# Optimization experiments

Measured on AMD Instinct MI355X. Metric: run time of the kernel, lower is better.

Reference implementation:

```python
import jax, jax.numpy as jnp
import numpy as np

N = 100000
IN_DIM = 128
OUT_DIM = 128
E = 320000


def setup_inputs() -> dict:
    key = jax.random.key(0)
    ks = jax.random.split(key, 12)
    x = jax.random.normal(ks[0], (N, IN_DIM), dtype=jnp.float32)
    src0 = jax.random.randint(ks[1], (E,), 0, N)
    dst0 = jax.random.randint(ks[2], (E,), 0, N)
    src1 = jax.random.randint(ks[3], (E,), 0, N)
    dst1 = jax.random.randint(ks[4], (E,), 0, N)
    s = 1.0 / np.sqrt(IN_DIM)
    W0 = jax.random.uniform(ks[5], (IN_DIM, OUT_DIM), minval=-s, maxval=s)
    b0 = jax.random.uniform(ks[6], (OUT_DIM,), minval=-s, maxval=s)
    W1 = jax.random.uniform(ks[7], (IN_DIM, OUT_DIM), minval=-s, maxval=s)
    b1 = jax.random.uniform(ks[8], (OUT_DIM,), minval=-s, maxval=s)
    sa = 1.0 / np.sqrt(2 * OUT_DIM)
    a0 = jax.random.uniform(ks[9], (2 * OUT_DIM,), minval=-sa, maxval=sa)
    a1 = jax.random.uniform(ks[10], (2 * OUT_DIM,), minval=-sa, maxval=sa)
    return {"x": x, "src0": src0, "dst0": dst0, "src1": src1, "dst1": dst1,
            "W0": W0, "b0": b0, "a0": a0, "W1": W1, "b1": b1, "a1": a1}


def _rel_gat(x, src, dst, W, b, a):
    # wh = Linear(in_dim, out_dim)(x)  -> [N, D]
    wh = x @ W + b
    D = wh.shape[1]
    # e = leaky_relu(a^T [wh_src || wh_dst]) ; split a instead of concat on edges
    e = jax.nn.leaky_relu(wh[src] @ a[:D] + wh[dst] @ a[D:])  # [E]
    # segment softmax over incoming edges of each dst node
    m = jax.ops.segment_max(e, dst, num_segments=N)
    ex = jnp.exp(e - m[dst])
    denom = jax.ops.segment_sum(ex, dst, num_segments=N)
    alpha = ex / denom[dst]  # [E]
    # weighted scatter-sum of src features (zero for isolated dst nodes)
    return jax.ops.segment_sum(alpha[:, None] * wh[src], dst, num_segments=N)


def reference(x, src0, dst0, src1, dst1, W0, b0, a0, W1, b1, a1):
    h0 = _rel_gat(x, src0, dst0, W0, b0, a0)
    h1 = _rel_gat(x, src1, dst1, W1, b1, a1)
    # cross-relation 'sum' reducer
    return h0 + h1
```

## Files before the change

### kernel.cpp

```cpp
#include <hip/hip_runtime.h>
#include <hip/hip_bf16.h>


typedef __bf16 bf16x8 __attribute__((ext_vector_type(8)));
typedef float f32x4 __attribute__((ext_vector_type(4)));

#define DIM 128
#define SPREAD 16

__global__ __launch_bounds__(256) void prep_w_kernel(
    const float* __restrict__ W0, const float* __restrict__ W1,
    __bf16* __restrict__ wtf)
{
    const int e = blockIdx.x * 256 + threadIdx.x;
    if (e >= 4096) return;
    const int lane = e & 63;
    const int ko4  = (e >> 6) & 3;
    const int ct   = (e >> 8) & 7;
    const int rel  = e >> 11;
    const float* W = rel ? W1 : W0;
    const int n  = ct * 16 + (lane & 15);
    const int k0 = ko4 * 32 + (lane >> 4) * 8;
    bf16x8 v;
#pragma unroll
    for (int j = 0; j < 8; ++j) v[j] = (__bf16)W[(k0 + j) * DIM + n];
    *(bf16x8*)(wtf + (size_t)e * 8) = v;
}

__global__ __launch_bounds__(256) void gemm_wh_kernel(
    const float* __restrict__ x, const __bf16* __restrict__ wtf,
    const float* __restrict__ b0, const float* __restrict__ b1,
    const float* __restrict__ a0, const float* __restrict__ a1,
    const int* __restrict__ dst0, const int* __restrict__ dst1,
    unsigned* __restrict__ deg, unsigned* __restrict__ rank,
    __bf16* __restrict__ wh, float* __restrict__ s_src,
    float* __restrict__ s_dst, int N, int E)
{
    __shared__ __align__(16) __bf16 Cst[64 * 136];
    const int tid = threadIdx.x;

    {
        const int gid = blockIdx.x * 256 + tid;
        if (gid < E) {
            rank[gid]     = atomicAdd(deg + (size_t)dst0[gid] * SPREAD, 1u);
            rank[E + gid] = atomicAdd(deg + ((size_t)N + dst1[gid]) * SPREAD, 1u);
        }
    }

    const int lane = tid & 63;
    const int wave = tid >> 6;
    const int quad = lane >> 4;
    const int mr   = lane & 15;

    const long row0 = (long)blockIdx.x * 64 + wave * 16;
    long arow = row0 + mr;
    if (arow >= N) arow = N - 1;
    const f32x4* xr = (const f32x4*)(x + arow * DIM);

    bf16x8 afrag[4];
#pragma unroll
    for (int ko4 = 0; ko4 < 4; ++ko4) {
        f32x4 lo = xr[ko4 * 8 + quad * 2], hi = xr[ko4 * 8 + quad * 2 + 1];
        afrag[ko4] = (bf16x8){ (__bf16)lo.x, (__bf16)lo.y, (__bf16)lo.z, (__bf16)lo.w,
                               (__bf16)hi.x, (__bf16)hi.y, (__bf16)hi.z, (__bf16)hi.w };
    }

    const bf16x8* wt = (const bf16x8*)wtf;

#pragma unroll
    for (int rel = 0; rel < 2; ++rel) {
        f32x4 zero = {0.f, 0.f, 0.f, 0.f};
        f32x4 acc[8];
#pragma unroll
        for (int t = 0; t < 8; ++t) acc[t] = zero;

#pragma unroll
        for (int ko4 = 0; ko4 < 4; ++ko4) {
#pragma unroll
            for (int ct = 0; ct < 8; ++ct) {
                bf16x8 bfrag = wt[((rel * 8 + ct) * 4 + ko4) * 64 + lane];
                acc[ct] = __builtin_amdgcn_mfma_f32_16x16x32_bf16(afrag[ko4], bfrag, acc[ct], 0, 0, 0);
            }
        }

        const float* bias = rel ? b1 : b0;
        const float* a    = rel ? a1 : a0;
        float psr[4] = {0.f, 0.f, 0.f, 0.f};
        float pdr[4] = {0.f, 0.f, 0.f, 0.f};
#pragma unroll
        for (int ct = 0; ct < 8; ++ct) {
            const int c = ct * 16 + mr;
            const float bn = bias[c];
            const float asc = a[c], adc = a[DIM + c];
#pragma unroll
            for (int rr = 0; rr < 4; ++rr) {
                const float wv = acc[ct][rr] + bn;
                Cst[(wave * 16 + quad * 4 + rr) * 136 + c] = (__bf16)wv;
                psr[rr] += asc * wv;
                pdr[rr] += adc * wv;
            }
        }
#pragma unroll
        for (int off = 1; off < 16; off <<= 1) {
#pragma unroll
            for (int rr = 0; rr < 4; ++rr) {
                psr[rr] += __shfl_xor(psr[rr], off);
                pdr[rr] += __shfl_xor(pdr[rr], off);
            }
        }
        if (mr == 0) {
#pragma unroll
            for (int rr = 0; rr < 4; ++rr) {
                const long orow = row0 + quad * 4 + rr;
                if (orow < N) {
                    s_src[(size_t)rel * N + orow] = psr[rr];
                    s_dst[(size_t)rel * N + orow] = pdr[rr];
                }
            }
        }
        __syncthreads();
#pragma unroll
        for (int i = 0; i < 4; ++i) {
            const int chunk = tid + 256 * i;
            const int row = chunk >> 4, c8 = chunk & 15;
            bf16x8 v = *(const bf16x8*)&Cst[row * 136 + c8 * 8];
            const long grow = (long)blockIdx.x * 64 + row;
            if (grow < N)
                *(bf16x8*)(wh + ((size_t)rel * N + grow) * DIM + c8 * 8) = v;
        }
        __syncthreads();
    }
}

__global__ __launch_bounds__(256) void scanA_kernel(
    const unsigned* __restrict__ deg, unsigned* __restrict__ tmp,
    unsigned* __restrict__ bsum, int n)
{
    __shared__ unsigned s[256];
    const int t = threadIdx.x;
    const int i = blockIdx.x * 256 + t;
    unsigned v = (i < n) ? deg[(size_t)i * SPREAD] : 0u;
    s[t] = v;
    __syncthreads();
#pragma unroll
    for (int off = 1; off < 256; off <<= 1) {
        unsigned add = (t >= off) ? s[t - off] : 0u;
        __syncthreads();
        s[t] += add;
        __syncthreads();
    }
    if (i < n) tmp[i] = s[t] - v;
    if (t == 255) bsum[blockIdx.x] = s[t];
}

__global__ __launch_bounds__(256) void scan2_kernel(
    const unsigned* __restrict__ tmp, const unsigned* __restrict__ bsum,
    const unsigned* __restrict__ deg, unsigned* __restrict__ rowptr,
    int n, int nb)
{
    __shared__ unsigned s[256];
    __shared__ unsigned ex[1024];
    const int t = threadIdx.x;
    unsigned loc[4], sum = 0u;
#pragma unroll
    for (int k = 0; k < 4; ++k) {
        int idx = t * 4 + k;
        loc[k] = (idx < nb) ? bsum[idx] : 0u;
        sum += loc[k];
    }
    s[t] = sum;
    __syncthreads();
#pragma unroll
    for (int off = 1; off < 256; off <<= 1) {
        unsigned add = (t >= off) ? s[t - off] : 0u;
        __syncthreads();
        s[t] += add;
        __syncthreads();
    }
    unsigned run = s[t] - sum;
#pragma unroll
    for (int k = 0; k < 4; ++k) {
        ex[t * 4 + k] = run;
        run += loc[k];
    }
    __syncthreads();
    const unsigned pref = ex[blockIdx.x];
    const int i = blockIdx.x * 256 + t;
    if (i < n) {
        unsigned val = tmp[i] + pref;
        rowptr[i] = val;
        if (i == n - 1) rowptr[n] = val + deg[(size_t)i * SPREAD];
    }
}

__global__ __launch_bounds__(256) void fill_kernel(
    const int* __restrict__ src0, const int* __restrict__ dst0,
    const int* __restrict__ src1, const int* __restrict__ dst1,
    const float* __restrict__ s_src, const float* __restrict__ s_dst,
    const unsigned* __restrict__ rowptr, const unsigned* __restrict__ rank,
    uint2* __restrict__ sorted, int N, int E)
{
    const int i = blockIdx.x * 256 + threadIdx.x;
    if (i >= E) return;
    const int s0 = src0[i], d0 = dst0[i];
    const int s1 = src1[i], d1 = dst1[i];
    const unsigned p0 = rowptr[d0] + rank[i];
    const unsigned p1 = rowptr[N + d1] + rank[E + i];

    float v0 = s_src[s0] + s_dst[d0];
    v0 = v0 > 0.f ? v0 : 0.01f * v0;
    const float e0 = __expf(v0);
    float v1 = s_src[N + s1] + s_dst[N + d1];
    v1 = v1 > 0.f ? v1 : 0.01f * v1;
    const float e1 = __expf(v1);

    sorted[p0] = make_uint2((unsigned)s0, __float_as_uint(e0));
    sorted[p1] = make_uint2((unsigned)s1, __float_as_uint(e1));
}

__global__ __launch_bounds__(256) void aggregate_kernel(
    const unsigned* __restrict__ rowptr, const uint2* __restrict__ sorted,
    const __bf16* __restrict__ wh, float* __restrict__ out, int N)
{
    const int tid  = threadIdx.x;
    const int lane = tid & 63;
    const int sub  = lane >> 4;
    const int mr   = lane & 15;
    int d = blockIdx.x * 4 + (tid >> 6);
    if (d >= N) return;
    d = __builtin_amdgcn_readfirstlane(d);

    const unsigned beg0 = rowptr[d],     end0 = rowptr[d + 1];
    const unsigned beg1 = rowptr[N + d], end1 = rowptr[N + d + 1];
    const unsigned len0 = end0 - beg0;
    const unsigned T    = len0 + (end1 - beg1);

    float acc0[8], acc1[8], l0 = 0.f, l1 = 0.f;
#pragma unroll
    for (int k = 0; k < 8; ++k) { acc0[k] = 0.f; acc1[k] = 0.f; }

    const size_t whstride = (size_t)N * DIM;

    for (unsigned t0 = 0; t0 < T; t0 += 8) {
        const unsigned tA = t0 + sub, tB = tA + 4;
        const bool vA = tA < T, vB = tB < T;
        const bool rA = tA >= len0, rB = tB >= len0;

        unsigned iA = rA ? beg1 + (tA - len0) : beg0 + tA;
        unsigned iB = rB ? beg1 + (tB - len0) : beg0 + tB;
        iA = vA ? iA : 0u;
        iB = vB ? iB : 0u;

        const uint2 eA = sorted[iA];
        const uint2 eB = sorted[iB];

        const float evA = vA ? __uint_as_float(eA.y) : 0.f;
        const float evB = vB ? __uint_as_float(eB.y) : 0.f;
        const float wA0 = rA ? 0.f : evA, wA1 = rA ? evA : 0.f;
        const float wB0 = rB ? 0.f : evB, wB1 = rB ? evB : 0.f;
        l0 += wA0 + wB0;
        l1 += wA1 + wB1;

        const bf16x8 wA = *(const bf16x8*)(wh + (rA ? whstride : 0)
                                              + (size_t)eA.x * DIM + mr * 8);
        const bf16x8 wB = *(const bf16x8*)(wh + (rB ? whstride : 0)
                                              + (size_t)eB.x * DIM + mr * 8);
#pragma unroll
        for (int k = 0; k < 8; ++k) {
            const float fA = (float)wA[k], fB = (float)wB[k];
            acc0[k] += wA0 * fA + wB0 * fB;
            acc1[k] += wA1 * fA + wB1 * fB;
        }
    }

#pragma unroll
    for (int k = 0; k < 8; ++k) {
        acc0[k] += __shfl_xor(acc0[k], 16);
        acc0[k] += __shfl_xor(acc0[k], 32);
        acc1[k] += __shfl_xor(acc1[k], 16);
        acc1[k] += __shfl_xor(acc1[k], 32);
    }
    l0 += __shfl_xor(l0, 16); l0 += __shfl_xor(l0, 32);
    l1 += __shfl_xor(l1, 16); l1 += __shfl_xor(l1, 32);

    const float inv0 = l0 > 0.f ? 1.f / l0 : 0.f;
    const float inv1 = l1 > 0.f ? 1.f / l1 : 0.f;

    if (sub == 0) {
        float o[8];
#pragma unroll
        for (int k = 0; k < 8; ++k) o[k] = acc0[k] * inv0 + acc1[k] * inv1;
        float4 v0 = {o[0], o[1], o[2], o[3]};
        float4 v1 = {o[4], o[5], o[6], o[7]};
        float* op = out + (size_t)d * DIM + mr * 8;
        *(float4*)op       = v0;
        *(float4*)(op + 4) = v1;
    }
}

extern "C" void kernel_launch(void* const* d_in, const int* in_sizes, int n_in,
                              void* d_out, int out_size, void* d_ws, size_t ws_size,
                              hipStream_t stream) {
    const float* x = (const float*)d_in[0];
    const int* srcs[2] = {(const int*)d_in[1], (const int*)d_in[3]};
    const int* dsts[2] = {(const int*)d_in[2], (const int*)d_in[4]};
    const float* Ws[2] = {(const float*)d_in[5], (const float*)d_in[8]};
    const float* Bs[2] = {(const float*)d_in[6], (const float*)d_in[9]};
    const float* As[2] = {(const float*)d_in[7], (const float*)d_in[10]};

    const int N = in_sizes[0] / DIM;
    const int E = in_sizes[1];
    const int n2 = 2 * N;
    const int nb = (n2 + 255) / 256;
    float* out = (float*)d_out;

    char* p = (char*)d_ws;
    __bf16*   wh     = (__bf16*)p;   p += (size_t)n2 * DIM * 2;
    __bf16*   wtf    = (__bf16*)p;   p += (size_t)4096 * 8 * 2;
    float*    s_src  = (float*)p;    p += (size_t)n2 * 4;
    float*    s_dst  = (float*)p;    p += (size_t)n2 * 4;
    unsigned* deg    = (unsigned*)p; p += (size_t)n2 * SPREAD * 4;
    unsigned* tmp    = (unsigned*)p; p += (size_t)n2 * 4;
    unsigned* rowptr = (unsigned*)p; p += (size_t)(n2 + 2) * 4;
    unsigned* rank   = (unsigned*)p; p += (size_t)2 * E * 4;
    uint2*    sorted = (uint2*)p;    p += (size_t)2 * E * 8;
    unsigned* bsum   = (unsigned*)p; p += (size_t)nb * 4;

    hipMemsetAsync(deg, 0, (size_t)n2 * SPREAD * 4, stream);
    prep_w_kernel<<<16, 256, 0, stream>>>(Ws[0], Ws[1], wtf);

    gemm_wh_kernel<<<(N + 63) / 64, 256, 0, stream>>>(
        x, wtf, Bs[0], Bs[1], As[0], As[1],
        dsts[0], dsts[1], deg, rank, wh, s_src, s_dst, N, E);

    scanA_kernel<<<nb, 256, 0, stream>>>(deg, tmp, bsum, n2);
    scan2_kernel<<<nb, 256, 0, stream>>>(tmp, bsum, deg, rowptr, n2, nb);
    fill_kernel<<<(E + 255) / 256, 256, 0, stream>>>(
        srcs[0], dsts[0], srcs[1], dsts[1], s_src, s_dst,
        rowptr, rank, sorted, N, E);
    aggregate_kernel<<<(N + 3) / 4, 256, 0, stream>>>(
        rowptr, sorted, wh, out, N);
}
```

Measured before the change: 232.2 us.

## Replace global atomic degree count with LDS-partitioned histogram feeder blocks

```diff
diff --git a/kernel.cpp b/kernel.cpp
--- a/kernel.cpp
+++ b/kernel.cpp
@@ -6,7 +6,10 @@
 typedef float f32x4 __attribute__((ext_vector_type(4)));
 
 #define DIM 128
-#define SPREAD 16
+#define NP 4
+#define NR 32
+#define FEEDER_BLOCKS (NP * NR)
+#define HIST_BINS 6400
 
 __global__ __launch_bounds__(256) void prep_w_kernel(
     const float* __restrict__ W0, const float* __restrict__ W1,
@@ -32,27 +35,59 @@
     const float* __restrict__ b0, const float* __restrict__ b1,
     const float* __restrict__ a0, const float* __restrict__ a1,
     const int* __restrict__ dst0, const int* __restrict__ dst1,
-    unsigned* __restrict__ deg, unsigned* __restrict__ rank,
+    unsigned* __restrict__ partial, unsigned* __restrict__ rank,
     __bf16* __restrict__ wh, float* __restrict__ s_src,
     float* __restrict__ s_dst, int N, int E)
 {
-    __shared__ __align__(16) __bf16 Cst[64 * 136];
+    __shared__ __align__(16) unsigned hist_[HIST_BINS];
     const int tid = threadIdx.x;
 
-    {
-        const int gid = blockIdx.x * 256 + tid;
-        if (gid < E) {
-            rank[gid]     = atomicAdd(deg + (size_t)dst0[gid] * SPREAD, 1u);
-            rank[E + gid] = atomicAdd(deg + ((size_t)N + dst1[gid]) * SPREAD, 1u);
-        }
-    }
+    if (blockIdx.x < FEEDER_BLOCKS) {
+        const int p    = blockIdx.x & (NP - 1);
+        const int r    = blockIdx.x >> 2;
+        const int rel  = r >> 4;
+        const int rr   = r & 15;
+        const int rngsz = (N + 15) / 16;
+        const int lo = rr * rngsz;
+        const int hi = min(lo + rngsz, N);
+        const int nbins = hi - lo;
+        for (int j = tid; j < nbins; j += 256) hist_[j] = 0u;
+        __syncthreads();
+
+        const int chunk = (E + NP - 1) / NP;
+        const int e0 = p * chunk;
+        const int e1 = min(e0 + chunk, E);
+        const int* dsts = rel ? dst1 : dst0;
+        unsigned* rk = rank + (rel ? E : 0);
+
+        for (int i = e0 + tid * 4; i < e1; i += 1024) {
+            if (i + 3 < e1) {
+                const int4 v = *(const int4*)(dsts + i);
+                if (v.x >= lo && v.x < hi) rk[i]     = atomicAdd(&hist_[v.x - lo], 1u);
+                if (v.y >= lo && v.y < hi) rk[i + 1] = atomicAdd(&hist_[v.y - lo], 1u);
+                if (v.z >= lo && v.z < hi) rk[i + 2] = atomicAdd(&hist_[v.z - lo], 1u);
+                if (v.w >= lo && v.w < hi) rk[i + 3] = atomicAdd(&hist_[v.w - lo], 1u);
+            } else {
+                for (int j = i; j < e1; ++j) {
+                    const int d = dsts[j];
+                    if (d >= lo && d < hi) rk[j] = atomicAdd(&hist_[d - lo], 1u);
+                }
+            }
+        }
+        __syncthreads();
+        unsigned* part = partial + (size_t)p * (2 * N) + (size_t)rel * N + lo;
+        for (int j = tid; j < nbins; j += 256) part[j] = hist_[j];
+        return;
+    }
+    const int bx = blockIdx.x - FEEDER_BLOCKS;
+    __bf16* Cst = (__bf16*)hist_;
 
     const int lane = tid & 63;
     const int wave = tid >> 6;
     const int quad = lane >> 4;
     const int mr   = lane & 15;
 
-    const long row0 = (long)blockIdx.x * 64 + wave * 16;
+    const long row0 = (long)bx * 64 + wave * 16;
     long arow = row0 + mr;
     if (arow >= N) arow = N - 1;
     const f32x4* xr = (const f32x4*)(x + arow * DIM);
@@ -124,7 +159,7 @@
             const int chunk = tid + 256 * i;
             const int row = chunk >> 4, c8 = chunk & 15;
             bf16x8 v = *(const bf16x8*)&Cst[row * 136 + c8 * 8];
-            const long grow = (long)blockIdx.x * 64 + row;
+            const long grow = (long)bx * 64 + row;
             if (grow < N)
                 *(bf16x8*)(wh + ((size_t)rel * N + grow) * DIM + c8 * 8) = v;
         }
@@ -133,13 +168,17 @@
 }
 
 __global__ __launch_bounds__(256) void scanA_kernel(
-    const unsigned* __restrict__ deg, unsigned* __restrict__ tmp,
+    const unsigned* __restrict__ partial, unsigned* __restrict__ tmp,
     unsigned* __restrict__ bsum, int n)
 {
     __shared__ unsigned s[256];
     const int t = threadIdx.x;
     const int i = blockIdx.x * 256 + t;
-    unsigned v = (i < n) ? deg[(size_t)i * SPREAD] : 0u;
+    unsigned v = 0u;
+    if (i < n) {
+#pragma unroll
+        for (int p = 0; p < NP; ++p) v += partial[(size_t)p * n + i];
+    }
     s[t] = v;
     __syncthreads();
 #pragma unroll
@@ -155,7 +194,7 @@
 
 __global__ __launch_bounds__(256) void scan2_kernel(
     const unsigned* __restrict__ tmp, const unsigned* __restrict__ bsum,
-    const unsigned* __restrict__ deg, unsigned* __restrict__ rowptr,
+    const unsigned* __restrict__ partial, unsigned* __restrict__ rowptr,
     int n, int nb)
 {
     __shared__ unsigned s[256];
@@ -189,7 +228,12 @@
     if (i < n) {
         unsigned val = tmp[i] + pref;
         rowptr[i] = val;
-        if (i == n - 1) rowptr[n] = val + deg[(size_t)i * SPREAD];
+        if (i == n - 1) {
+            unsigned dsum = 0u;
+#pragma unroll
+            for (int p = 0; p < NP; ++p) dsum += partial[(size_t)p * n + i];
+            rowptr[n] = val + dsum;
+        }
     }
 }
 
@@ -198,14 +242,24 @@
     const int* __restrict__ src1, const int* __restrict__ dst1,
     const float* __restrict__ s_src, const float* __restrict__ s_dst,
     const unsigned* __restrict__ rowptr, const unsigned* __restrict__ rank,
+    const unsigned* __restrict__ partial,
     uint2* __restrict__ sorted, int N, int E)
 {
     const int i = blockIdx.x * 256 + threadIdx.x;
     if (i >= E) return;
     const int s0 = src0[i], d0 = dst0[i];
     const int s1 = src1[i], d1 = dst1[i];
-    const unsigned p0 = rowptr[d0] + rank[i];
-    const unsigned p1 = rowptr[N + d1] + rank[E + i];
+
+    const int chunk = (E + NP - 1) / NP;
+    const int p = i / chunk;
+    const int n2 = 2 * N;
+    unsigned off0 = 0u, off1 = 0u;
+    for (int q = 0; q < p; ++q) {
+        off0 += partial[(size_t)q * n2 + d0];
+        off1 += partial[(size_t)q * n2 + N + d1];
+    }
+    const unsigned p0 = rowptr[d0] + off0 + rank[i];
+    const unsigned p1 = rowptr[N + d1] + off1 + rank[E + i];
 
     float v0 = s_src[s0] + s_dst[d0];
     v0 = v0 > 0.f ? v0 : 0.01f * v0;
@@ -315,29 +369,28 @@
     float* out = (float*)d_out;
 
     char* p = (char*)d_ws;
-    __bf16*   wh     = (__bf16*)p;   p += (size_t)n2 * DIM * 2;
-    __bf16*   wtf    = (__bf16*)p;   p += (size_t)4096 * 8 * 2;
-    float*    s_src  = (float*)p;    p += (size_t)n2 * 4;
-    float*    s_dst  = (float*)p;    p += (size_t)n2 * 4;
-    unsigned* deg    = (unsigned*)p; p += (size_t)n2 * SPREAD * 4;
-    unsigned* tmp    = (unsigned*)p; p += (size_t)n2 * 4;
-    unsigned* rowptr = (unsigned*)p; p += (size_t)(n2 + 2) * 4;
-    unsigned* rank   = (unsigned*)p; p += (size_t)2 * E * 4;
-    uint2*    sorted = (uint2*)p;    p += (size_t)2 * E * 8;
-    unsigned* bsum   = (unsigned*)p; p += (size_t)nb * 4;
-
-    hipMemsetAsync(deg, 0, (size_t)n2 * SPREAD * 4, stream);
+    __bf16*   wh      = (__bf16*)p;   p += (size_t)n2 * DIM * 2;
+    __bf16*   wtf     = (__bf16*)p;   p += (size_t)4096 * 8 * 2;
+    float*    s_src   = (float*)p;    p += (size_t)n2 * 4;
+    float*    s_dst   = (float*)p;    p += (size_t)n2 * 4;
+    unsigned* partial = (unsigned*)p; p += (size_t)NP * n2 * 4;
+    unsigned* tmp     = (unsigned*)p; p += (size_t)n2 * 4;
+    unsigned* rowptr  = (unsigned*)p; p += (size_t)(n2 + 2) * 4;
+    unsigned* rank    = (unsigned*)p; p += (size_t)2 * E * 4;
+    uint2*    sorted  = (uint2*)p;    p += (size_t)2 * E * 8;
+    unsigned* bsum    = (unsigned*)p; p += (size_t)nb * 4;
+
     prep_w_kernel<<<16, 256, 0, stream>>>(Ws[0], Ws[1], wtf);
 
-    gemm_wh_kernel<<<(N + 63) / 64, 256, 0, stream>>>(
+    gemm_wh_kernel<<<FEEDER_BLOCKS + (N + 63) / 64, 256, 0, stream>>>(
         x, wtf, Bs[0], Bs[1], As[0], As[1],
-        dsts[0], dsts[1], deg, rank, wh, s_src, s_dst, N, E);
-
-    scanA_kernel<<<nb, 256, 0, stream>>>(deg, tmp, bsum, n2);
-    scan2_kernel<<<nb, 256, 0, stream>>>(tmp, bsum, deg, rowptr, n2, nb);
+        dsts[0], dsts[1], partial, rank, wh, s_src, s_dst, N, E);
+
+    scanA_kernel<<<nb, 256, 0, stream>>>(partial, tmp, bsum, n2);
+    scan2_kernel<<<nb, 256, 0, stream>>>(tmp, bsum, partial, rowptr, n2, nb);
     fill_kernel<<<(E + 255) / 256, 256, 0, stream>>>(
         srcs[0], dsts[0], srcs[1], dsts[1], s_src, s_dst,
-        rowptr, rank, sorted, N, E);
+        rowptr, rank, partial, sorted, N, E);
     aggregate_kernel<<<(N + 3) / 4, 256, 0, stream>>>(
         rowptr, sorted, wh, out, N);
 }
```

New measurement: 244.9 us. 5.4% more time.
